# Kernel tuning notes

Measured on AMD Instinct MI355X. Metric: run time of the kernel, lower is better.

The kernel has to match this reference:

```python
import jax, jax.numpy as jnp
import numpy as np

N = 100000      # active input voxels (== output voxels, stride=1)
K = 27          # kernel volume: 3**3 hypercube offsets
M = 50000       # active in/out pairs per kernel offset
CIN = 64
COUT = 64


def setup_inputs() -> dict:
    key = jax.random.key(0)
    k1, k2, k3, k4 = jax.random.split(key, 4)
    std = (2.0 / CIN / K) ** 0.5
    x = jax.random.normal(k1, (N, CIN), dtype=jnp.float32)
    kernel = jax.random.normal(k2, (K, CIN, COUT), dtype=jnp.float32) * std
    bias = jnp.zeros((1, COUT), dtype=jnp.float32)
    in_map = jax.random.randint(k3, (K, M), 0, N, dtype=jnp.int64)
    out_map = jax.random.randint(k4, (K, M), 0, N, dtype=jnp.int64)
    return {"x": x, "kernel": kernel, "bias": bias,
            "in_map": in_map, "out_map": out_map}


def reference(x, kernel, bias, in_map, out_map):
    # Sparse voxel convolution: per kernel-offset gather -> matmul -> scatter-add.
    gathered = x[in_map]                                   # [K, M, Cin]
    prod = jnp.einsum('kmc,kcd->kmd', gathered, kernel)    # [K, M, Cout]
    out = jnp.zeros((N, COUT), dtype=x.dtype)
    out = out.at[out_map.reshape(-1)].add(prod.reshape(-1, COUT))
    out = out + bias                                       # bias is [1, Cout]
    return out
```

## Files before the change

kernel.cpp:

```cpp
#include <hip/hip_runtime.h>

#define N_VOX 100000
#define KVOL 27
#define MPAIR 50000
#define CIN 64
#define COUT 64
#define TILES_PER_WAVE 8
#define NTILES 3125

typedef __attribute__((ext_vector_type(8))) short bf16x8;
typedef __attribute__((ext_vector_type(4))) float f32x4;

__device__ inline short f2bf(float f) {
    union { float f; unsigned u; } v; v.f = f;
    return (short)((v.u + 0x7FFFu + ((v.u >> 16) & 1u)) >> 16);
}

__global__ void spconv_init_bias(const float* __restrict__ bias,
                                 float* __restrict__ out, int total) {
    int i = blockIdx.x * blockDim.x + threadIdx.x;
    if (i < total) out[i] = bias[i & (COUT - 1)];
}

__global__ __launch_bounds__(256) void spconv_mfma(
    const float* __restrict__ x,
    const float* __restrict__ kern,
    const int*   __restrict__ in_map,
    const int*   __restrict__ out_map,
    float*       __restrict__ out)
{
    const int lane = threadIdx.x & 63;
    const int wave = threadIdx.x >> 6;
    const int k    = blockIdx.y;
    const int g    = lane >> 4;
    const int r16  = lane & 15;

    bf16x8 bfrag[2][4];
    {
        const float* wp = kern + (size_t)k * CIN * COUT;
        #pragma unroll
        for (int s = 0; s < 2; ++s)
            #pragma unroll
            for (int t = 0; t < 4; ++t) {
                const float* p = wp + (s * 32 + g * 8) * COUT + t * 16 + r16;
                bf16x8 f;
                #pragma unroll
                for (int j = 0; j < 8; ++j) f[j] = f2bf(p[j * COUT]);
                bfrag[s][t] = f;
            }
    }

    for (int it = 0; it < TILES_PER_WAVE; ++it) {
        int tile = (blockIdx.x * 4 + wave) * TILES_PER_WAVE + it;
        if (tile >= NTILES) break;
        int base = k * MPAIR + tile * 16;

        int im = in_map[base + r16];

        bf16x8 afrag[2];
        const float* xp = x + (size_t)im * CIN + g * 8;
        #pragma unroll
        for (int s = 0; s < 2; ++s) {
            f32x4 v0 = *(const f32x4*)(xp + s * 32);
            f32x4 v1 = *(const f32x4*)(xp + s * 32 + 4);
            bf16x8 f;
            f[0] = f2bf(v0[0]); f[1] = f2bf(v0[1]);
            f[2] = f2bf(v0[2]); f[3] = f2bf(v0[3]);
            f[4] = f2bf(v1[0]); f[5] = f2bf(v1[1]);
            f[6] = f2bf(v1[2]); f[7] = f2bf(v1[3]);
            afrag[s] = f;
        }

        f32x4 acc[4] = {{0.f,0.f,0.f,0.f},{0.f,0.f,0.f,0.f},
                        {0.f,0.f,0.f,0.f},{0.f,0.f,0.f,0.f}};
        #pragma unroll
        for (int t = 0; t < 4; ++t) {
            acc[t] = __builtin_amdgcn_mfma_f32_16x16x32_bf16(afrag[0], bfrag[0][t], acc[t], 0, 0, 0);
            acc[t] = __builtin_amdgcn_mfma_f32_16x16x32_bf16(afrag[1], bfrag[1][t], acc[t], 0, 0, 0);
        }

        int orow[4];
        #pragma unroll
        for (int r = 0; r < 4; ++r) orow[r] = out_map[base + g * 4 + r];
        #pragma unroll
        for (int r = 0; r < 4; ++r) {
            float* op = out + (size_t)orow[r] * COUT + r16;
            #pragma unroll
            for (int t = 0; t < 4; ++t)
                atomicAdd(op + t * 16, acc[t][r]);
        }
    }
}

extern "C" void kernel_launch(void* const* d_in, const int* in_sizes, int n_in,
                              void* d_out, int out_size, void* d_ws, size_t ws_size,
                              hipStream_t stream) {
    const float* x       = (const float*)d_in[0];
    const float* kern    = (const float*)d_in[1];
    const float* bias    = (const float*)d_in[2];
    const int*   in_map  = (const int*)d_in[3];
    const int*   out_map = (const int*)d_in[4];
    float*       out     = (float*)d_out;

    int total = N_VOX * COUT;
    spconv_init_bias<<<(total + 255) / 256, 256, 0, stream>>>(bias, out, total);

    dim3 grid((NTILES + 4 * TILES_PER_WAVE - 1) / (4 * TILES_PER_WAVE), KVOL);
    spconv_mfma<<<grid, 256, 0, stream>>>(x, kern, in_map, out_map, out);
}
```

Before: 364.2 us.

## Accumulate scatter-add in fp16 workspace with packed half2 atomics

Moves the scatter accumulation into a zeroed fp16 workspace and uses packed half2 atomic adds, with lane pairs exchanging values through shuffles to form the pairs. This halves the number of atomic operations and the bytes they touch. A finalize kernel converts the workspace back to fp32 and adds the bias. Summing in fp16 loses precision and adds two extra passes over the output, and the fp32-atomic path is kept as a fallback when the workspace is too small.

```diff
diff --git a/kernel.cpp b/kernel.cpp
--- a/kernel.cpp
+++ b/kernel.cpp
@@ -1,4 +1,5 @@
 #include <hip/hip_runtime.h>
+#include <hip/hip_fp16.h>
 
 #define N_VOX 100000
 #define KVOL 27
@@ -16,13 +17,110 @@
     return (short)((v.u + 0x7FFFu + ((v.u >> 16) & 1u)) >> 16);
 }
 
+
+__global__ void spconv_zero_ws(__half2* __restrict__ ws, int n2) {
+    int i = blockIdx.x * blockDim.x + threadIdx.x;
+    if (i < n2) ws[i] = __float2half2_rn(0.f);
+}
+
+__global__ void spconv_finalize(const __half2* __restrict__ ws,
+                                const float* __restrict__ bias,
+                                float* __restrict__ out, int n2) {
+    int i = blockIdx.x * blockDim.x + threadIdx.x;
+    if (i >= n2) return;
+    float2 v = __half22float2(ws[i]);
+    int c2 = (i & (COUT / 2 - 1)) * 2;
+    float2 o; o.x = v.x + bias[c2]; o.y = v.y + bias[c2 + 1];
+    ((float2*)out)[i] = o;
+}
+
+__global__ __launch_bounds__(256) void spconv_mfma_f16ws(
+    const float* __restrict__ x,
+    const float* __restrict__ kern,
+    const int*   __restrict__ in_map,
+    const int*   __restrict__ out_map,
+    __half2*     __restrict__ ws)
+{
+    const int lane = threadIdx.x & 63;
+    const int wave = threadIdx.x >> 6;
+    const int k    = blockIdx.y;
+    const int g    = lane >> 4;
+    const int r16  = lane & 15;
+    const int p    = r16 & 1;
+
+    bf16x8 bfrag[2][4];
+    {
+        const float* wp = kern + (size_t)k * CIN * COUT;
+        #pragma unroll
+        for (int s = 0; s < 2; ++s)
+            #pragma unroll
+            for (int t = 0; t < 4; ++t) {
+                const float* q = wp + (s * 32 + g * 8) * COUT + t * 16 + r16;
+                bf16x8 f;
+                #pragma unroll
+                for (int j = 0; j < 8; ++j) f[j] = f2bf(q[j * COUT]);
+                bfrag[s][t] = f;
+            }
+    }
+
+    for (int it = 0; it < TILES_PER_WAVE; ++it) {
+        int tile = (blockIdx.x * 4 + wave) * TILES_PER_WAVE + it;
+        if (tile >= NTILES) break;
+        int base = k * MPAIR + tile * 16;
+
+        int im = in_map[base + r16];
+        bf16x8 afrag[2];
+        const float* xp = x + (size_t)im * CIN + g * 8;
+        #pragma unroll
+        for (int s = 0; s < 2; ++s) {
+            f32x4 v0 = *(const f32x4*)(xp + s * 32);
+            f32x4 v1 = *(const f32x4*)(xp + s * 32 + 4);
+            bf16x8 f;
+            f[0] = f2bf(v0[0]); f[1] = f2bf(v0[1]);
+            f[2] = f2bf(v0[2]); f[3] = f2bf(v0[3]);
+            f[4] = f2bf(v1[0]); f[5] = f2bf(v1[1]);
+            f[6] = f2bf(v1[2]); f[7] = f2bf(v1[3]);
+            afrag[s] = f;
+        }
+
+        f32x4 acc[4] = {{0.f,0.f,0.f,0.f},{0.f,0.f,0.f,0.f},
+                        {0.f,0.f,0.f,0.f},{0.f,0.f,0.f,0.f}};
+        #pragma unroll
+        for (int t = 0; t < 4; ++t) {
+            acc[t] = __builtin_amdgcn_mfma_f32_16x16x32_bf16(afrag[0], bfrag[0][t], acc[t], 0, 0, 0);
+            acc[t] = __builtin_amdgcn_mfma_f32_16x16x32_bf16(afrag[1], bfrag[1][t], acc[t], 0, 0, 0);
+        }
+
+        int orow[4];
+        #pragma unroll
+        for (int r = 0; r < 4; ++r) orow[r] = out_map[base + g * 4 + r];
+
+        #pragma unroll
+        for (int r = 0; r < 4; ++r) {
+            float pv[4];
+            #pragma unroll
+            for (int t = 0; t < 4; ++t) pv[t] = __shfl_xor(acc[t][r], 1);
+            __half2* wrow = ws + (size_t)orow[r] * (COUT / 2);
+            #pragma unroll
+            for (int q = 0; q < 2; ++q) {
+                int t = 2 * p + q;
+                float lo = p ? pv[t] : acc[t][r];
+                float hi = p ? acc[t][r] : pv[t];
+                int col = t * 16 + r16 - p;
+                unsafeAtomicAdd(wrow + (col >> 1), __floats2half2_rn(lo, hi));
+            }
+        }
+    }
+}
+
+
 __global__ void spconv_init_bias(const float* __restrict__ bias,
                                  float* __restrict__ out, int total) {
     int i = blockIdx.x * blockDim.x + threadIdx.x;
     if (i < total) out[i] = bias[i & (COUT - 1)];
 }
 
-__global__ __launch_bounds__(256) void spconv_mfma(
+__global__ __launch_bounds__(256) void spconv_mfma_f32at(
     const float* __restrict__ x,
     const float* __restrict__ kern,
     const int*   __restrict__ in_map,
@@ -42,10 +140,10 @@
         for (int s = 0; s < 2; ++s)
             #pragma unroll
             for (int t = 0; t < 4; ++t) {
-                const float* p = wp + (s * 32 + g * 8) * COUT + t * 16 + r16;
+                const float* q = wp + (s * 32 + g * 8) * COUT + t * 16 + r16;
                 bf16x8 f;
                 #pragma unroll
-                for (int j = 0; j < 8; ++j) f[j] = f2bf(p[j * COUT]);
+                for (int j = 0; j < 8; ++j) f[j] = f2bf(q[j * COUT]);
                 bfrag[s][t] = f;
             }
     }
@@ -56,7 +154,6 @@
         int base = k * MPAIR + tile * 16;
 
         int im = in_map[base + r16];
-
         bf16x8 afrag[2];
         const float* xp = x + (size_t)im * CIN + g * 8;
         #pragma unroll
@@ -102,9 +199,18 @@
     const int*   out_map = (const int*)d_in[4];
     float*       out     = (float*)d_out;
 
-    int total = N_VOX * COUT;
-    spconv_init_bias<<<(total + 255) / 256, 256, 0, stream>>>(bias, out, total);
-
     dim3 grid((NTILES + 4 * TILES_PER_WAVE - 1) / (4 * TILES_PER_WAVE), KVOL);
-    spconv_mfma<<<grid, 256, 0, stream>>>(x, kern, in_map, out_map, out);
-}
+
+    const size_t ws_need = (size_t)N_VOX * COUT * sizeof(__half);
+    if (ws_size >= ws_need) {
+        __half2* ws = (__half2*)d_ws;
+        int n2 = N_VOX * COUT / 2;
+        spconv_zero_ws<<<(n2 + 255) / 256, 256, 0, stream>>>(ws, n2);
+        spconv_mfma_f16ws<<<grid, 256, 0, stream>>>(x, kern, in_map, out_map, ws);
+        spconv_finalize<<<(n2 + 255) / 256, 256, 0, stream>>>(ws, bias, out, n2);
+    } else {
+        int total = N_VOX * COUT;
+        spconv_init_bias<<<(total + 255) / 256, 256, 0, stream>>>(bias, out, total);
+        spconv_mfma_f32at<<<grid, 256, 0, stream>>>(x, kern, in_map, out_map, out);
+    }
+}
```

Measured after the change: 369.0 us. About the same (+1.3%).

## Pre-convert x to bf16 in workspace and software-pipeline gathers

Applied to the files above, without the earlier changes.

Adds a pre-pass that converts x to bf16 into the workspace, so the main kernel gathers half as many bytes per row and skips per-gather conversion. The main kernel preloads all in_map indices for its tiles and double-buffers the next tile's A fragment and out_map rows while computing the current tile, to hide gather latency. It costs an extra kernel launch and a full pass over x. The original fp32 path is kept as a fallback when the workspace is too small.

```diff
diff --git a/kernel.cpp b/kernel.cpp
--- a/kernel.cpp
+++ b/kernel.cpp
@@ -5,15 +5,16 @@
 #define MPAIR 50000
 #define CIN 64
 #define COUT 64
-#define TILES_PER_WAVE 8
+#define TPW 8
 #define NTILES 3125
 
 typedef __attribute__((ext_vector_type(8))) short bf16x8;
 typedef __attribute__((ext_vector_type(4))) float f32x4;
-
-__device__ inline short f2bf(float f) {
+typedef __attribute__((ext_vector_type(4))) unsigned short u16x4;
+
+__device__ inline unsigned short f2bf(float f) {
     union { float f; unsigned u; } v; v.f = f;
-    return (short)((v.u + 0x7FFFu + ((v.u >> 16) & 1u)) >> 16);
+    return (unsigned short)((v.u + 0x7FFFu + ((v.u >> 16) & 1u)) >> 16);
 }
 
 __global__ void spconv_init_bias(const float* __restrict__ bias,
@@ -22,7 +23,100 @@
     if (i < total) out[i] = bias[i & (COUT - 1)];
 }
 
-__global__ __launch_bounds__(256) void spconv_mfma(
+__global__ void spconv_x_to_bf16(const float* __restrict__ x,
+                                 unsigned short* __restrict__ xbf, int n4) {
+    int i = blockIdx.x * blockDim.x + threadIdx.x;
+    if (i >= n4) return;
+    f32x4 v = ((const f32x4*)x)[i];
+    u16x4 o; o.x = f2bf(v.x); o.y = f2bf(v.y); o.z = f2bf(v.z); o.w = f2bf(v.w);
+    ((u16x4*)xbf)[i] = o;
+}
+
+__global__ __launch_bounds__(256) void spconv_mfma_pipe(
+    const unsigned short* __restrict__ xbf,
+    const float* __restrict__ kern,
+    const int*   __restrict__ in_map,
+    const int*   __restrict__ out_map,
+    float*       __restrict__ out)
+{
+    const int lane = threadIdx.x & 63;
+    const int wave = threadIdx.x >> 6;
+    const int k    = blockIdx.y;
+    const int g    = lane >> 4;
+    const int r16  = lane & 15;
+
+    bf16x8 bfrag[2][4];
+    {
+        const float* wp = kern + (size_t)k * CIN * COUT;
+        #pragma unroll
+        for (int s = 0; s < 2; ++s)
+            #pragma unroll
+            for (int t = 0; t < 4; ++t) {
+                const float* q = wp + (s * 32 + g * 8) * COUT + t * 16 + r16;
+                bf16x8 f;
+                #pragma unroll
+                for (int j = 0; j < 8; ++j) f[j] = (short)f2bf(q[j * COUT]);
+                bfrag[s][t] = f;
+            }
+    }
+
+    const int tile0 = (blockIdx.x * 4 + wave) * TPW;
+    const int base0 = k * MPAIR;
+
+    int inrow[TPW];
+    #pragma unroll
+    for (int t = 0; t < TPW; ++t) {
+        int tl = tile0 + t; tl = tl < NTILES ? tl : NTILES - 1;
+        inrow[t] = in_map[base0 + tl * 16 + r16];
+    }
+
+    bf16x8 acur[2], anxt[2];
+    #pragma unroll
+    for (int s = 0; s < 2; ++s)
+        acur[s] = *(const bf16x8*)(xbf + (size_t)inrow[0] * CIN + g * 8 + s * 32);
+
+    int orow_c[4], orow_n[4];
+    {
+        int tl = tile0 < NTILES ? tile0 : NTILES - 1;
+        #pragma unroll
+        for (int r = 0; r < 4; ++r) orow_c[r] = out_map[base0 + tl * 16 + g * 4 + r];
+    }
+
+    #pragma unroll
+    for (int t = 0; t < TPW; ++t) {
+        if (t + 1 < TPW) {
+            int tl = tile0 + t + 1; tl = tl < NTILES ? tl : NTILES - 1;
+            #pragma unroll
+            for (int s = 0; s < 2; ++s)
+                anxt[s] = *(const bf16x8*)(xbf + (size_t)inrow[t + 1] * CIN + g * 8 + s * 32);
+            #pragma unroll
+            for (int r = 0; r < 4; ++r) orow_n[r] = out_map[base0 + tl * 16 + g * 4 + r];
+        }
+
+        if (tile0 + t < NTILES) {
+            f32x4 acc[4] = {{0.f,0.f,0.f,0.f},{0.f,0.f,0.f,0.f},
+                            {0.f,0.f,0.f,0.f},{0.f,0.f,0.f,0.f}};
+            #pragma unroll
+            for (int q = 0; q < 4; ++q) {
+                acc[q] = __builtin_amdgcn_mfma_f32_16x16x32_bf16(acur[0], bfrag[0][q], acc[q], 0, 0, 0);
+                acc[q] = __builtin_amdgcn_mfma_f32_16x16x32_bf16(acur[1], bfrag[1][q], acc[q], 0, 0, 0);
+            }
+            #pragma unroll
+            for (int r = 0; r < 4; ++r) {
+                float* op = out + (size_t)orow_c[r] * COUT + r16;
+                #pragma unroll
+                for (int q = 0; q < 4; ++q)
+                    atomicAdd(op + q * 16, acc[q][r]);
+            }
+        }
+
+        acur[0] = anxt[0]; acur[1] = anxt[1];
+        #pragma unroll
+        for (int r = 0; r < 4; ++r) orow_c[r] = orow_n[r];
+    }
+}
+
+__global__ __launch_bounds__(256) void spconv_mfma_f32at(
     const float* __restrict__ x,
     const float* __restrict__ kern,
     const int*   __restrict__ in_map,
@@ -42,21 +136,20 @@
         for (int s = 0; s < 2; ++s)
             #pragma unroll
             for (int t = 0; t < 4; ++t) {
-                const float* p = wp + (s * 32 + g * 8) * COUT + t * 16 + r16;
+                const float* q = wp + (s * 32 + g * 8) * COUT + t * 16 + r16;
                 bf16x8 f;
                 #pragma unroll
-                for (int j = 0; j < 8; ++j) f[j] = f2bf(p[j * COUT]);
+                for (int j = 0; j < 8; ++j) f[j] = (short)f2bf(q[j * COUT]);
                 bfrag[s][t] = f;
             }
     }
 
-    for (int it = 0; it < TILES_PER_WAVE; ++it) {
-        int tile = (blockIdx.x * 4 + wave) * TILES_PER_WAVE + it;
+    for (int it = 0; it < TPW; ++it) {
+        int tile = (blockIdx.x * 4 + wave) * TPW + it;
         if (tile >= NTILES) break;
         int base = k * MPAIR + tile * 16;
 
         int im = in_map[base + r16];
-
         bf16x8 afrag[2];
         const float* xp = x + (size_t)im * CIN + g * 8;
         #pragma unroll
@@ -64,19 +157,19 @@
             f32x4 v0 = *(const f32x4*)(xp + s * 32);
             f32x4 v1 = *(const f32x4*)(xp + s * 32 + 4);
             bf16x8 f;
-            f[0] = f2bf(v0[0]); f[1] = f2bf(v0[1]);
-            f[2] = f2bf(v0[2]); f[3] = f2bf(v0[3]);
-            f[4] = f2bf(v1[0]); f[5] = f2bf(v1[1]);
-            f[6] = f2bf(v1[2]); f[7] = f2bf(v1[3]);
+            f[0] = (short)f2bf(v0[0]); f[1] = (short)f2bf(v0[1]);
+            f[2] = (short)f2bf(v0[2]); f[3] = (short)f2bf(v0[3]);
+            f[4] = (short)f2bf(v1[0]); f[5] = (short)f2bf(v1[1]);
+            f[6] = (short)f2bf(v1[2]); f[7] = (short)f2bf(v1[3]);
             afrag[s] = f;
         }
 
         f32x4 acc[4] = {{0.f,0.f,0.f,0.f},{0.f,0.f,0.f,0.f},
                         {0.f,0.f,0.f,0.f},{0.f,0.f,0.f,0.f}};
         #pragma unroll
-        for (int t = 0; t < 4; ++t) {
-            acc[t] = __builtin_amdgcn_mfma_f32_16x16x32_bf16(afrag[0], bfrag[0][t], acc[t], 0, 0, 0);
-            acc[t] = __builtin_amdgcn_mfma_f32_16x16x32_bf16(afrag[1], bfrag[1][t], acc[t], 0, 0, 0);
+        for (int q = 0; q < 4; ++q) {
+            acc[q] = __builtin_amdgcn_mfma_f32_16x16x32_bf16(afrag[0], bfrag[0][q], acc[q], 0, 0, 0);
+            acc[q] = __builtin_amdgcn_mfma_f32_16x16x32_bf16(afrag[1], bfrag[1][q], acc[q], 0, 0, 0);
         }
 
         int orow[4];
@@ -86,8 +179,8 @@
         for (int r = 0; r < 4; ++r) {
             float* op = out + (size_t)orow[r] * COUT + r16;
             #pragma unroll
-            for (int t = 0; t < 4; ++t)
-                atomicAdd(op + t * 16, acc[t][r]);
+            for (int q = 0; q < 4; ++q)
+                atomicAdd(op + q * 16, acc[q][r]);
         }
     }
 }
@@ -102,9 +195,18 @@
     const int*   out_map = (const int*)d_in[4];
     float*       out     = (float*)d_out;
 
+    dim3 grid((NTILES + 4 * TPW - 1) / (4 * TPW), KVOL);
+
     int total = N_VOX * COUT;
     spconv_init_bias<<<(total + 255) / 256, 256, 0, stream>>>(bias, out, total);
 
-    dim3 grid((NTILES + 4 * TILES_PER_WAVE - 1) / (4 * TILES_PER_WAVE), KVOL);
-    spconv_mfma<<<grid, 256, 0, stream>>>(x, kern, in_map, out_map, out);
-}
+    const size_t ws_need = (size_t)N_VOX * CIN * sizeof(unsigned short);
+    if (ws_size >= ws_need) {
+        unsigned short* xbf = (unsigned short*)d_ws;
+        int n4 = N_VOX * CIN / 4;
+        spconv_x_to_bf16<<<(n4 + 255) / 256, 256, 0, stream>>>(x, xbf, n4);
+        spconv_mfma_pipe<<<grid, 256, 0, stream>>>(xbf, kern, in_map, out_map, out);
+    } else {
+        spconv_mfma_f32at<<<grid, 256, 0, stream>>>(x, kern, in_map, out_map, out);
+    }
+}
```

New measurement: 369.5 us. No clear change (+1.5%).
